# Performance work log

Hardware: AMD Instinct MI355X
Metric: run time of the kernel (lower is better)

The kernel has to match this reference:

```python
import jax, jax.numpy as jnp
import numpy as np

NUM_HEADS = 12
KSIZE = 3
PAD = 1


def setup_inputs() -> dict:
    key = jax.random.key(0)
    ks = jax.random.split(key, 5)
    B, H, W, C = 4, 96, 96, 192
    x = jax.random.normal(ks[0], (B, H * W, C), jnp.float32)
    Wq = jax.random.normal(ks[1], (W, W), jnp.float32) * 0.02
    bq = jnp.zeros((W,), jnp.float32)
    Wkv = jax.random.normal(ks[2], (2 * W, W), jnp.float32) * 0.02
    bkv = jnp.zeros((2 * W,), jnp.float32)
    Wp = jax.random.normal(ks[3], (C, C), jnp.float32) * 0.02
    bp = jnp.zeros((C,), jnp.float32)
    f_qr = jnp.float32(1.0)
    f_kr = jnp.float32(1.0)
    f_vr = jnp.float32(1.0)
    return {"x": x, "Wq": Wq, "bq": bq, "Wkv": Wkv, "bkv": bkv, "Wp": Wp,
            "bp": bp, "f_qr": f_qr, "f_kr": f_kr, "f_vr": f_vr, "H": H, "W": W}


def reference(x, Wq, bq, Wkv, bkv, Wp, bp, f_qr, f_kr, f_vr, H, W):
    B, N, C = x.shape
    nh = NUM_HEADS
    hc = C // nh
    scale = C ** (-0.5)
    # faithful to torch: raw reshape of (B, N, C) into (B, C, H, W)
    xn = x.reshape(B, C, H, W)
    # q_proj is Linear over the last (width) axis, size Hw == W
    q = jnp.einsum('bchw,vw->bchv', xn, Wq) + bq            # (B,C,H,W)
    q = q.reshape(B, H, W, nh, hc).transpose(0, 3, 1, 2, 4)  # (B,nh,H,W,hc)
    q = (q * scale * f_qr).reshape(B, nh, H * W, hc)         # (B,nh,L,hc)
    # kv_proj: Linear(W -> 2W) over last axis
    kv = jnp.einsum('bchw,vw->bchv', xn, Wkv) + bkv          # (B,C,H,2W)
    kv = kv.reshape(B, H, W, 2, nh, hc).transpose(3, 0, 4, 5, 1, 2)  # (2,B,nh,hc,H,W)
    kv = jnp.pad(kv, ((0, 0),) * 4 + ((PAD, PAD), (PAD, PAD)))       # zero-pad spatial
    # unfold: 3x3 sliding windows, stride 1 -> one window per pixel
    patches = jnp.stack([kv[..., i:i + H, j:j + W]
                         for i in range(KSIZE) for j in range(KSIZE)], axis=4)
    # (2,B,nh,hc,9,H,W) -> (2,B,nh,L,9,hc); kernel index = kh*3+kw matches nn.Unfold
    patches = patches.reshape(2, B, nh, hc, KSIZE * KSIZE, H * W).transpose(0, 1, 2, 5, 4, 3)
    k = patches[0] * f_kr                                    # (B,nh,L,9,hc)
    v = patches[1] * f_vr
    attn = jax.nn.softmax(jnp.einsum('bnlc,bnlkc->bnlk', q, k), axis=-1)  # (B,nh,L,9)
    out = jnp.einsum('bnlk,bnlkc->bnlc', attn, v)            # (B,nh,L,hc)
    out = out.transpose(0, 2, 1, 3).reshape(B, H, W, C)      # (B,H,W,C)
    out = jnp.einsum('bhwc,oc->bhwo', out, Wp) + bp          # proj Linear(dim,dim)
    return out.reshape(B, H * W, C)
```

## Files before the change

### kernel.cpp

```cpp
#include <hip/hip_runtime.h>

#define HW2   96
#define NH    12
#define LPIX  (HW2*HW2)
#define BATCH 4

typedef __attribute__((ext_vector_type(8))) short bf16x8;
typedef __attribute__((ext_vector_type(4))) float f32x4;

static __device__ __forceinline__ float bf2f(unsigned short u) {
  union { unsigned int i; float f; } v; v.i = ((unsigned int)u) << 16; return v.f;
}
static __device__ __forceinline__ unsigned short f2bf(float f) {
  union { float f; unsigned int i; } v; v.f = f;
  unsigned int r = v.i + 0x7FFF + ((v.i >> 16) & 1);
  return (unsigned short)(r >> 16);
}

__global__ __launch_bounds__(256) void cvt_w_kernel(
    const float* __restrict__ Wq, const float* __restrict__ Wkv,
    const float* __restrict__ Wp,
    unsigned short* __restrict__ wqb, unsigned short* __restrict__ wkvb,
    unsigned short* __restrict__ wpb) {
  int i = blockIdx.x * 256 + threadIdx.x;
  if (i < 9216)       wqb[i]          = f2bf(Wq[i]);
  else if (i < 27648) wkvb[i - 9216]  = f2bf(Wkv[i - 9216]);
  else if (i < 64512) wpb[i - 27648]  = f2bf(Wp[i - 27648]);
}

__global__ __launch_bounds__(256) void qkv_gemm(
    const float* __restrict__ X,
    const unsigned short* __restrict__ wq, const unsigned short* __restrict__ wkv,
    const float* __restrict__ bq, const float* __restrict__ bkv,
    const float* __restrict__ fqr, const float* __restrict__ fkr,
    const float* __restrict__ fvr,
    unsigned short* __restrict__ Qb, unsigned short* __restrict__ KVb)
{
  const int tid  = threadIdx.x;
  const int r0   = blockIdx.x * 128;
  const int lane = tid & 63, w = tid >> 6;
  const int col  = lane & 15;
  const int koff = (lane >> 4) * 8;
  const int arow0 = r0 + 16 * w + (lane & 15);
  const int rb0   = r0 + 16 * w + 4 * (lane >> 4);

  bf16x8 af[2][3];
  #pragma unroll
  for (int t = 0; t < 2; t++) {
    const float* xr = X + (size_t)(arow0 + 64 * t) * 96;
    float xv[24];
    *(float4*)&xv[0]  = *(const float4*)(xr + koff);
    *(float4*)&xv[4]  = *(const float4*)(xr + koff + 4);
    *(float4*)&xv[8]  = *(const float4*)(xr + koff + 32);
    *(float4*)&xv[12] = *(const float4*)(xr + koff + 36);
    *(float4*)&xv[16] = *(const float4*)(xr + koff + 64);
    *(float4*)&xv[20] = *(const float4*)(xr + koff + 68);
    unsigned short au[24];
    #pragma unroll
    for (int j = 0; j < 24; j++) au[j] = f2bf(xv[j]);
    af[t][0] = *(const bf16x8*)&au[0];
    af[t][1] = *(const bf16x8*)&au[8];
    af[t][2] = *(const bf16x8*)&au[16];
  }

  const float fqr0 = fqr[0] * 0.07216878364870322f;
  const float fkr0 = fkr[0], fvr0 = fvr[0];

  #pragma unroll
  for (int g = 0; g < 6; g++) {
    bf16x8 bw0[3], bw1[3], bw2[3];
    #pragma unroll
    for (int j = 0; j < 3; j++) {
      int nt = g * 3 + j;
      const unsigned short* wrow = (nt < 6)
          ? wq  + (size_t)(nt * 16 + col) * 96 + koff
          : wkv + (size_t)((nt - 6) * 16 + col) * 96 + koff;
      bw0[j] = *(const bf16x8*)(wrow);
      bw1[j] = *(const bf16x8*)(wrow + 32);
      bw2[j] = *(const bf16x8*)(wrow + 64);
    }
    asm volatile("" ::: "memory");

    #pragma unroll
    for (int j = 0; j < 3; j++) {
      int nt = g * 3 + j;
      f32x4 acc[2];
      #pragma unroll
      for (int t = 0; t < 2; t++) {
        f32x4 a = {0.f, 0.f, 0.f, 0.f};
        a = __builtin_amdgcn_mfma_f32_16x16x32_bf16(af[t][0], bw0[j], a, 0, 0, 0);
        a = __builtin_amdgcn_mfma_f32_16x16x32_bf16(af[t][1], bw1[j], a, 0, 0, 0);
        a = __builtin_amdgcn_mfma_f32_16x16x32_bf16(af[t][2], bw2[j], a, 0, 0, 0);
        acc[t] = a;
      }

      if (nt < 6) {
        int u = nt * 16 + col;
        float bias = bq[u];
        #pragma unroll
        for (int t = 0; t < 2; t++)
          #pragma unroll
          for (int i = 0; i < 4; i++)
            Qb[(size_t)(rb0 + 64 * t + i) * 96 + u] = f2bf((acc[t][i] + bias) * fqr0);
      } else {
        int u = (nt - 6) * 16 + col;
        float bias = bkv[u];
        #pragma unroll
        for (int t = 0; t < 2; t++)
          #pragma unroll
          for (int i = 0; i < 4; i++) {
            float s = (i & 1) ? fvr0 : fkr0;
            KVb[(size_t)(rb0 + 64 * t + i) * 192 + u] = f2bf((acc[t][i] + bias) * s);
          }
      }
    }
  }
}

__global__ __launch_bounds__(384) void attnproj_kernel(
    const unsigned short* __restrict__ Qb, const unsigned short* __restrict__ KVb,
    const unsigned short* __restrict__ wp, const float* __restrict__ bp,
    float* __restrict__ Out)
{
  __shared__ unsigned short s_out[64 * 204];
  const int tid = threadIdx.x;
  const int bid = (blockIdx.x & 7) * 72 + (blockIdx.x >> 3);
  const int bl0 = bid * 64;

  {
    const int n  = tid % NH;
    const int pp = tid / NH;
    const int b  = bl0 / LPIX;
    const int l0 = (bl0 % LPIX) + 2 * pp;
    const int h2 = l0 / HW2, w2 = l0 - h2 * HW2;

    const unsigned short* kvb = KVb + (size_t)b * (LPIX * 384) + n * 16;

    int nbo[12];
    #pragma unroll
    for (int hx = 0; hx < 12; hx++) {
      int hh = h2 + hx / 4 - 1;
      int ww = w2 + (hx & 3) - 1;
      int hc = min(max(hh, 0), HW2 - 1);
      int wc = min(max(ww, 0), HW2 - 1);
      nbo[hx] = (hc * HW2 + wc) * 384;
    }
    const bool rok[3] = { h2 > 0, true, h2 < HW2 - 1 };

    uint4 kH[12][2];
    #pragma unroll
    for (int hx = 0; hx < 12; hx++) {
      const unsigned short* kp = kvb + nbo[hx];
      kH[hx][0] = *(const uint4*)(kp);
      kH[hx][1] = *(const uint4*)(kp + 8);
    }
    uint4 qA[2], qB[2];
    #pragma unroll
    for (int t = 0; t < 2; t++) {
      const unsigned short* qp = Qb + (size_t)(b * LPIX + l0 + t) * 192 + n * 16;
      qA[t] = *(const uint4*)(qp);
      qB[t] = *(const uint4*)(qp + 8);
    }
    asm volatile("" ::: "memory");

    float q[2][16];
    #pragma unroll
    for (int t = 0; t < 2; t++) {
      const unsigned short* qs = (const unsigned short*)&qA[t];
      #pragma unroll
      for (int j = 0; j < 8; j++) q[t][j] = bf2f(qs[j]);
      qs = (const unsigned short*)&qB[t];
      #pragma unroll
      for (int j = 0; j < 8; j++) q[t][8 + j] = bf2f(qs[j]);
    }

    float sc[2][9];
    bool  okk[2][9];
    #pragma unroll
    for (int t = 0; t < 2; t++) {
      #pragma unroll
      for (int kk = 0; kk < 9; kk++) {
        int dr = kk / 3, dc = kk % 3;
        int hx = dr * 4 + dc + t;
        int wcol = w2 + t + dc - 1;
        okk[t][kk] = rok[dr] && ((unsigned)wcol < (unsigned)HW2);
        float s = 0.f;
        const unsigned short* kd = (const unsigned short*)&kH[hx][0];
        #pragma unroll
        for (int j = 0; j < 8; j++) s = fmaf(q[t][j], bf2f(kd[j]), s);
        kd = (const unsigned short*)&kH[hx][1];
        #pragma unroll
        for (int j = 0; j < 8; j++) s = fmaf(q[t][8 + j], bf2f(kd[j]), s);
        sc[t][kk] = okk[t][kk] ? s : 0.f;
      }
    }

    uint4 vH[12][2];
    #pragma unroll
    for (int hx = 0; hx < 12; hx++) {
      const unsigned short* vp = kvb + nbo[hx] + 192;
      vH[hx][0] = *(const uint4*)(vp);
      vH[hx][1] = *(const uint4*)(vp + 8);
    }
    asm volatile("" ::: "memory");

    #pragma unroll
    for (int t = 0; t < 2; t++) {
      float m = sc[t][0];
      #pragma unroll
      for (int kk = 1; kk < 9; kk++) m = fmaxf(m, sc[t][kk]);
      float ssum = 0.f;
      #pragma unroll
      for (int kk = 0; kk < 9; kk++) {
        float e = __expf(sc[t][kk] - m);
        sc[t][kk] = e;
        ssum += e;
      }
      float acc[16];
      #pragma unroll
      for (int j = 0; j < 16; j++) acc[j] = 0.f;
      #pragma unroll
      for (int kk = 0; kk < 9; kk++) {
        int hx = (kk / 3) * 4 + (kk % 3) + t;
        float wgt = okk[t][kk] ? sc[t][kk] : 0.f;
        const unsigned short* vd = (const unsigned short*)&vH[hx][0];
        #pragma unroll
        for (int j = 0; j < 8; j++) acc[j] = fmaf(wgt, bf2f(vd[j]), acc[j]);
        vd = (const unsigned short*)&vH[hx][1];
        #pragma unroll
        for (int j = 0; j < 8; j++) acc[8 + j] = fmaf(wgt, bf2f(vd[j]), acc[8 + j]);
      }
      float rinv = 1.f / ssum;
      unsigned short od[16];
      #pragma unroll
      for (int j = 0; j < 16; j++) od[j] = f2bf(acc[j] * rinv);
      unsigned short* op = s_out + (2 * pp + t) * 204 + n * 16;
      *(uint4*)(op)     = *(uint4*)&od[0];
      *(uint4*)(op + 8) = *(uint4*)&od[8];
    }
  }
  __syncthreads();

  const int lane = tid & 63, w = tid >> 6;
  const int wr = w & 1, wh = w >> 1;
  const int col  = lane & 15;
  const int koff = (lane >> 4) * 8;

  bf16x8 af[2][6];
  #pragma unroll
  for (int rg = 0; rg < 2; rg++) {
    int arow = 32 * wr + 16 * rg + (lane & 15);
    #pragma unroll
    for (int kt = 0; kt < 6; kt++)
      af[rg][kt] = *(const bf16x8*)&s_out[arow * 204 + koff + kt * 32];
  }

  #pragma unroll
  for (int t4 = 0; t4 < 4; t4++) {
    int nt = wh * 4 + t4;
    const unsigned short* wrow = wp + (size_t)(nt * 16 + col) * 192 + koff;
    bf16x8 bw[6];
    #pragma unroll
    for (int kt = 0; kt < 6; kt++) bw[kt] = *(const bf16x8*)(wrow + kt * 32);
    asm volatile("" ::: "memory");

    int u = nt * 16 + col;
    float bias = bp[u];
    #pragma unroll
    for (int rg = 0; rg < 2; rg++) {
      f32x4 acc = {0.f, 0.f, 0.f, 0.f};
      #pragma unroll
      for (int kt = 0; kt < 6; kt++)
        acc = __builtin_amdgcn_mfma_f32_16x16x32_bf16(af[rg][kt], bw[kt], acc, 0, 0, 0);
      int rbase = bl0 + 32 * wr + 16 * rg + 4 * (lane >> 4);
      #pragma unroll
      for (int i = 0; i < 4; i++)
        Out[(size_t)(rbase + i) * 192 + u] = acc[i] + bias;
    }
  }
}

extern "C" void kernel_launch(void* const* d_in, const int* in_sizes, int n_in,
                              void* d_out, int out_size, void* d_ws, size_t ws_size,
                              hipStream_t stream) {
  const float* x   = (const float*)d_in[0];
  const float* Wq  = (const float*)d_in[1];
  const float* bq  = (const float*)d_in[2];
  const float* Wkv = (const float*)d_in[3];
  const float* bkv = (const float*)d_in[4];
  const float* Wp  = (const float*)d_in[5];
  const float* bp  = (const float*)d_in[6];
  const float* fqr = (const float*)d_in[7];
  const float* fkr = (const float*)d_in[8];
  const float* fvr = (const float*)d_in[9];

  char* ws = (char*)d_ws;
  unsigned short* Qb   = (unsigned short*)ws;
  unsigned short* KVb  = (unsigned short*)(ws + 14155776);
  unsigned short* wqb  = (unsigned short*)(ws + 42467328);
  unsigned short* wkvb = (unsigned short*)(ws + 42485760);
  unsigned short* wpb  = (unsigned short*)(ws + 42522624);

  cvt_w_kernel<<<dim3(252), dim3(256), 0, stream>>>(Wq, Wkv, Wp, wqb, wkvb, wpb);

  qkv_gemm<<<dim3(576), dim3(256), 0, stream>>>(
      x, wqb, wkvb, bq, bkv, fqr, fkr, fvr, Qb, KVb);

  attnproj_kernel<<<dim3(576), dim3(384), 0, stream>>>(
      Qb, KVb, wpb, bp, (float*)d_out);
}
```

Measured before the change: 64.91 us.

## Tile attention per thread as 2x2 pixel block to reuse 4x4 K/V halo

Each thread now computes a 2x2 pixel patch (two rows, two columns) instead of two adjacent pixels. It loads a 4x4 K/V neighbourhood, so 16 halo loads serve 4 pixels where 12 previously served 2, cutting redundant global traffic. Blocks cover 2 rows by 32 columns with 192 threads, and each projection wave handles 4 row groups. The cost is more registers per thread (launch bounds 192,1) and fewer threads per block, which may lower occupancy and latency hiding.

```diff
diff --git a/kernel.cpp b/kernel.cpp
--- a/kernel.cpp
+++ b/kernel.cpp
@@ -117,7 +117,7 @@
   }
 }
 
-__global__ __launch_bounds__(384) void attnproj_kernel(
+__global__ __launch_bounds__(192, 1) void attnproj_kernel(
     const unsigned short* __restrict__ Qb, const unsigned short* __restrict__ KVb,
     const unsigned short* __restrict__ wp, const float* __restrict__ bp,
     float* __restrict__ Out)
@@ -125,79 +125,79 @@
   __shared__ unsigned short s_out[64 * 204];
   const int tid = threadIdx.x;
   const int bid = (blockIdx.x & 7) * 72 + (blockIdx.x >> 3);
-  const int bl0 = bid * 64;
+  const int b   = bid / 144;
+  const int rem = bid % 144;
+  const int hp  = rem / 3, wt = rem % 3;
+  const int h   = 2 * hp;
+  const int w0  = 32 * wt;
 
   {
     const int n  = tid % NH;
-    const int pp = tid / NH;
-    const int b  = bl0 / LPIX;
-    const int l0 = (bl0 % LPIX) + 2 * pp;
-    const int h2 = l0 / HW2, w2 = l0 - h2 * HW2;
+    const int qd = tid / NH;
+    const int w  = w0 + 2 * qd;
 
     const unsigned short* kvb = KVb + (size_t)b * (LPIX * 384) + n * 16;
 
-    int nbo[12];
-    #pragma unroll
-    for (int hx = 0; hx < 12; hx++) {
-      int hh = h2 + hx / 4 - 1;
-      int ww = w2 + (hx & 3) - 1;
+    int nbo[16];
+    #pragma unroll
+    for (int hx = 0; hx < 16; hx++) {
+      int hh = h + (hx >> 2) - 1;
+      int ww = w + (hx & 3) - 1;
       int hc = min(max(hh, 0), HW2 - 1);
       int wc = min(max(ww, 0), HW2 - 1);
       nbo[hx] = (hc * HW2 + wc) * 384;
     }
-    const bool rok[3] = { h2 > 0, true, h2 < HW2 - 1 };
-
-    uint4 kH[12][2];
-    #pragma unroll
-    for (int hx = 0; hx < 12; hx++) {
+    const bool rok[4] = { h > 0, true, true, h < HW2 - 2 };
+
+    uint4 kH[16][2];
+    #pragma unroll
+    for (int hx = 0; hx < 16; hx++) {
       const unsigned short* kp = kvb + nbo[hx];
       kH[hx][0] = *(const uint4*)(kp);
       kH[hx][1] = *(const uint4*)(kp + 8);
     }
-    uint4 qA[2], qB[2];
-    #pragma unroll
-    for (int t = 0; t < 2; t++) {
-      const unsigned short* qp = Qb + (size_t)(b * LPIX + l0 + t) * 192 + n * 16;
+    uint4 qA[4], qB[4];
+    #pragma unroll
+    for (int t = 0; t < 4; t++) {
+      int l = (h + (t >> 1)) * HW2 + w + (t & 1);
+      const unsigned short* qp = Qb + ((size_t)b * LPIX + l) * 192 + n * 16;
       qA[t] = *(const uint4*)(qp);
       qB[t] = *(const uint4*)(qp + 8);
     }
     asm volatile("" ::: "memory");
 
-    float q[2][16];
-    #pragma unroll
-    for (int t = 0; t < 2; t++) {
+    float sc[4][9];
+    bool  okk[4][9];
+    #pragma unroll
+    for (int t = 0; t < 4; t++) {
+      const int tr = t >> 1, tc = t & 1;
+      float q[16];
       const unsigned short* qs = (const unsigned short*)&qA[t];
       #pragma unroll
-      for (int j = 0; j < 8; j++) q[t][j] = bf2f(qs[j]);
+      for (int j = 0; j < 8; j++) q[j] = bf2f(qs[j]);
       qs = (const unsigned short*)&qB[t];
       #pragma unroll
-      for (int j = 0; j < 8; j++) q[t][8 + j] = bf2f(qs[j]);
-    }
-
-    float sc[2][9];
-    bool  okk[2][9];
-    #pragma unroll
-    for (int t = 0; t < 2; t++) {
+      for (int j = 0; j < 8; j++) q[8 + j] = bf2f(qs[j]);
       #pragma unroll
       for (int kk = 0; kk < 9; kk++) {
         int dr = kk / 3, dc = kk % 3;
-        int hx = dr * 4 + dc + t;
-        int wcol = w2 + t + dc - 1;
-        okk[t][kk] = rok[dr] && ((unsigned)wcol < (unsigned)HW2);
+        int hx = (dr + tr) * 4 + dc + tc;
+        int wcol = w + tc + dc - 1;
+        okk[t][kk] = rok[dr + tr] && ((unsigned)wcol < (unsigned)HW2);
         float s = 0.f;
         const unsigned short* kd = (const unsigned short*)&kH[hx][0];
         #pragma unroll
-        for (int j = 0; j < 8; j++) s = fmaf(q[t][j], bf2f(kd[j]), s);
+        for (int j = 0; j < 8; j++) s = fmaf(q[j], bf2f(kd[j]), s);
         kd = (const unsigned short*)&kH[hx][1];
         #pragma unroll
-        for (int j = 0; j < 8; j++) s = fmaf(q[t][8 + j], bf2f(kd[j]), s);
+        for (int j = 0; j < 8; j++) s = fmaf(q[8 + j], bf2f(kd[j]), s);
         sc[t][kk] = okk[t][kk] ? s : 0.f;
       }
     }
 
-    uint4 vH[12][2];
-    #pragma unroll
-    for (int hx = 0; hx < 12; hx++) {
+    uint4 vH[16][2];
+    #pragma unroll
+    for (int hx = 0; hx < 16; hx++) {
       const unsigned short* vp = kvb + nbo[hx] + 192;
       vH[hx][0] = *(const uint4*)(vp);
       vH[hx][1] = *(const uint4*)(vp + 8);
@@ -205,7 +205,8 @@
     asm volatile("" ::: "memory");
 
     #pragma unroll
-    for (int t = 0; t < 2; t++) {
+    for (int t = 0; t < 4; t++) {
+      const int tr = t >> 1, tc = t & 1;
       float m = sc[t][0];
       #pragma unroll
       for (int kk = 1; kk < 9; kk++) m = fmaxf(m, sc[t][kk]);
@@ -221,7 +222,7 @@
       for (int j = 0; j < 16; j++) acc[j] = 0.f;
       #pragma unroll
       for (int kk = 0; kk < 9; kk++) {
-        int hx = (kk / 3) * 4 + (kk % 3) + t;
+        int hx = (kk / 3 + tr) * 4 + kk % 3 + tc;
         float wgt = okk[t][kk] ? sc[t][kk] : 0.f;
         const unsigned short* vd = (const unsigned short*)&vH[hx][0];
         #pragma unroll
@@ -234,22 +235,22 @@
       unsigned short od[16];
       #pragma unroll
       for (int j = 0; j < 16; j++) od[j] = f2bf(acc[j] * rinv);
-      unsigned short* op = s_out + (2 * pp + t) * 204 + n * 16;
+      int sr = tr * 32 + 2 * qd + tc;
+      unsigned short* op = s_out + sr * 204 + n * 16;
       *(uint4*)(op)     = *(uint4*)&od[0];
       *(uint4*)(op + 8) = *(uint4*)&od[8];
     }
   }
   __syncthreads();
 
-  const int lane = tid & 63, w = tid >> 6;
-  const int wr = w & 1, wh = w >> 1;
+  const int lane = tid & 63, wv = tid >> 6;
   const int col  = lane & 15;
   const int koff = (lane >> 4) * 8;
 
-  bf16x8 af[2][6];
+  bf16x8 af[4][6];
   #pragma unroll
-  for (int rg = 0; rg < 2; rg++) {
-    int arow = 32 * wr + 16 * rg + (lane & 15);
+  for (int rg = 0; rg < 4; rg++) {
+    int arow = 16 * rg + (lane & 15);
     #pragma unroll
     for (int kt = 0; kt < 6; kt++)
       af[rg][kt] = *(const bf16x8*)&s_out[arow * 204 + koff + kt * 32];
@@ -257,7 +258,7 @@
 
   #pragma unroll
   for (int t4 = 0; t4 < 4; t4++) {
-    int nt = wh * 4 + t4;
+    int nt = wv * 4 + t4;
     const unsigned short* wrow = wp + (size_t)(nt * 16 + col) * 192 + koff;
     bf16x8 bw[6];
     #pragma unroll
@@ -267,15 +268,18 @@
     int u = nt * 16 + col;
     float bias = bp[u];
     #pragma unroll
-    for (int rg = 0; rg < 2; rg++) {
+    for (int rg = 0; rg < 4; rg++) {
       f32x4 acc = {0.f, 0.f, 0.f, 0.f};
       #pragma unroll
       for (int kt = 0; kt < 6; kt++)
         acc = __builtin_amdgcn_mfma_f32_16x16x32_bf16(af[rg][kt], bw[kt], acc, 0, 0, 0);
-      int rbase = bl0 + 32 * wr + 16 * rg + 4 * (lane >> 4);
-      #pragma unroll
-      for (int i = 0; i < 4; i++)
-        Out[(size_t)(rbase + i) * 192 + u] = acc[i] + bias;
+      int hh_out = h + (rg >> 1);
+      int wbase  = w0 + 16 * (rg & 1) + 4 * (lane >> 4);
+      #pragma unroll
+      for (int i = 0; i < 4; i++) {
+        int row_g = b * LPIX + hh_out * HW2 + wbase + i;
+        Out[(size_t)row_g * 192 + u] = acc[i] + bias;
+      }
     }
   }
 }
@@ -306,6 +310,6 @@
   qkv_gemm<<<dim3(576), dim3(256), 0, stream>>>(
       x, wqb, wkvb, bq, bkv, fqr, fkr, fvr, Qb, KVb);
 
-  attnproj_kernel<<<dim3(576), dim3(384), 0, stream>>>(
+  attnproj_kernel<<<dim3(576), dim3(192), 0, stream>>>(
       Qb, KVb, wpb, bp, (float*)d_out);
 }
```

After: 63.82 us, median of 3. Within noise of the previous version (-1.7%).
